# Performance work log

Measured on AMD Instinct MI355X. Metric: run time of the kernel, lower is better.

## Reference

```python
import jax, jax.numpy as jnp
import numpy as np


def setup_inputs() -> dict:
    key = jax.random.key(0)
    ks = jax.random.split(key, 4)
    B, T, I, H, O = 1024, 512, 64, 128, 10
    return {
        "x": jax.random.normal(ks[0], (B, T, I), dtype=jnp.float32),
        "W_hx": jax.random.normal(ks[1], (H, I), dtype=jnp.float32) * (6.0 / (H + I)) ** 0.5,
        "W_hh": jax.random.normal(ks[2], (H, H), dtype=jnp.float32) * (6.0 / (H + H)) ** 0.5,
        "b_hh": jnp.zeros((H,), dtype=jnp.float32),
        "W_ph": jax.random.normal(ks[3], (O, H), dtype=jnp.float32) * (6.0 / (O + H)) ** 0.5,
        "b_ph": jnp.zeros((O,), dtype=jnp.float32),
    }


def reference(x, W_hx, W_hh, b_hh, W_ph, b_ph):
    B, T, I = x.shape
    H = W_hh.shape[0]
    # Precompute input projections for all timesteps in one GEMM: [B,T,H]
    xproj = jnp.einsum("bti,hi->bth", x, W_hx)
    h0 = jnp.zeros((B, H), dtype=x.dtype)

    def step(h, xp_t):
        # xp_t: [B,H]; recurrent update h = tanh(W_hx x_t + W_hh h + b)
        h_new = jnp.tanh(xp_t + h @ W_hh.T + b_hh)
        return h_new, None

    # scan over time (leading axis): xproj transposed to [T,B,H]
    h_T, _ = jax.lax.scan(step, h0, jnp.swapaxes(xproj, 0, 1))
    return h_T @ W_ph.T + b_ph
```

## Files before the change

kernel.cpp:

```cpp
#include <hip/hip_runtime.h>
#include <math.h>


#define T_STEPS 512
#define I_DIM   64
#define H_DIM   128
#define O_DIM   10
#define BT      16
#define PITCH   136

typedef short  bf16x8 __attribute__((ext_vector_type(8)));
typedef float  f32x4  __attribute__((ext_vector_type(4)));

static __device__ inline short f2bf(float f) {
    union { float f; unsigned u; } v; v.f = f;
    unsigned r = v.u + 0x7FFFu + ((v.u >> 16) & 1u);
    return (short)(r >> 16);
}
static __device__ inline float bf2f(short s) {
    union { unsigned u; float f; } v; v.u = ((unsigned)(unsigned short)s) << 16;
    return v.f;
}

static __device__ inline void lds_barrier() {
    asm volatile("s_waitcnt lgkmcnt(0)\n\ts_barrier" ::: "memory");
}

#define RNN_STEP(t, XR)                                                         \
    {                                                                           \
        const int p = (t) & 1;                                                  \
         \
        const short* hb = hbuf[p] + c * PITCH + q * 8;                          \
        bf16x8 Ah0 = *(const bf16x8*)(hb +  0);                                 \
        bf16x8 Ah1 = *(const bf16x8*)(hb + 32);                                 \
        bf16x8 Ah2 = *(const bf16x8*)(hb + 64);                                 \
        bf16x8 Ah3 = *(const bf16x8*)(hb + 96);                                 \
          \
          \
        bf16x8 Ax0, Ax1;                                                        \
        Ax0[0]=f2bf(XR[0].x); Ax0[1]=f2bf(XR[0].y); Ax0[2]=f2bf(XR[0].z); Ax0[3]=f2bf(XR[0].w); \
        Ax0[4]=f2bf(XR[1].x); Ax0[5]=f2bf(XR[1].y); Ax0[6]=f2bf(XR[1].z); Ax0[7]=f2bf(XR[1].w); \
        Ax1[0]=f2bf(XR[2].x); Ax1[1]=f2bf(XR[2].y); Ax1[2]=f2bf(XR[2].z); Ax1[3]=f2bf(XR[2].w); \
        Ax1[4]=f2bf(XR[3].x); Ax1[5]=f2bf(XR[3].y); Ax1[6]=f2bf(XR[3].z); Ax1[7]=f2bf(XR[3].w); \
        {                                                                       \
            const int tn = ((t) + 2 < T_STEPS) ? (t) + 2 : T_STEPS - 1;         \
            const float* pn = xrow + (size_t)tn * I_DIM;                        \
            XR[0] = *(const float4*)(pn +      q * 8);                          \
            XR[1] = *(const float4*)(pn +      q * 8 + 4);                      \
            XR[2] = *(const float4*)(pn + 32 + q * 8);                          \
            XR[3] = *(const float4*)(pn + 32 + q * 8 + 4);                      \
        }                                                                       \
            \
        f32x4 C0a = {0.f,0.f,0.f,0.f}, C0b = {0.f,0.f,0.f,0.f};                 \
        f32x4 C1a = {0.f,0.f,0.f,0.f}, C1b = {0.f,0.f,0.f,0.f};                 \
        C0a = __builtin_amdgcn_mfma_f32_16x16x32_bf16(Ax0, __builtin_bit_cast(bf16x8, Bw[0][4]), C0a, 0, 0, 0); \
        C1a = __builtin_amdgcn_mfma_f32_16x16x32_bf16(Ax0, __builtin_bit_cast(bf16x8, Bw[1][4]), C1a, 0, 0, 0); \
        C0b = __builtin_amdgcn_mfma_f32_16x16x32_bf16(Ax1, __builtin_bit_cast(bf16x8, Bw[0][5]), C0b, 0, 0, 0); \
        C1b = __builtin_amdgcn_mfma_f32_16x16x32_bf16(Ax1, __builtin_bit_cast(bf16x8, Bw[1][5]), C1b, 0, 0, 0); \
        C0a = __builtin_amdgcn_mfma_f32_16x16x32_bf16(Ah0, __builtin_bit_cast(bf16x8, Bw[0][0]), C0a, 0, 0, 0); \
        C1a = __builtin_amdgcn_mfma_f32_16x16x32_bf16(Ah0, __builtin_bit_cast(bf16x8, Bw[1][0]), C1a, 0, 0, 0); \
        C0b = __builtin_amdgcn_mfma_f32_16x16x32_bf16(Ah1, __builtin_bit_cast(bf16x8, Bw[0][1]), C0b, 0, 0, 0); \
        C1b = __builtin_amdgcn_mfma_f32_16x16x32_bf16(Ah1, __builtin_bit_cast(bf16x8, Bw[1][1]), C1b, 0, 0, 0); \
        C0a = __builtin_amdgcn_mfma_f32_16x16x32_bf16(Ah2, __builtin_bit_cast(bf16x8, Bw[0][2]), C0a, 0, 0, 0); \
        C1a = __builtin_amdgcn_mfma_f32_16x16x32_bf16(Ah2, __builtin_bit_cast(bf16x8, Bw[1][2]), C1a, 0, 0, 0); \
        C0b = __builtin_amdgcn_mfma_f32_16x16x32_bf16(Ah3, __builtin_bit_cast(bf16x8, Bw[0][3]), C0b, 0, 0, 0); \
        C1b = __builtin_amdgcn_mfma_f32_16x16x32_bf16(Ah3, __builtin_bit_cast(bf16x8, Bw[1][3]), C1b, 0, 0, 0); \
        const f32x4 C0 = C0a + C0b;                                             \
        const f32x4 C1 = C1a + C1b;                                             \
              \
        short* hw = hbuf[1 - p];                                                \
        _Pragma("unroll")                                                       \
        for (int r = 0; r < 4; ++r) {                                           \
            const int m = q * 4 + r;                                            \
            float s0 = C0[r] + bias0;                                           \
            float s1 = C1[r] + bias1;                                           \
            float e0 = __builtin_amdgcn_exp2f(s0 * 2.885390081777926825f);      \
            float e1 = __builtin_amdgcn_exp2f(s1 * 2.885390081777926825f);      \
            float h0 = fmaf(-2.0f, __builtin_amdgcn_rcpf(e0 + 1.0f), 1.0f);     \
            float h1 = fmaf(-2.0f, __builtin_amdgcn_rcpf(e1 + 1.0f), 1.0f);     \
            hw[m * PITCH + w * 32 + c]      = f2bf(h0);                         \
            hw[m * PITCH + w * 32 + 16 + c] = f2bf(h1);                         \
        }                                                                       \
        lds_barrier();               \
    }

__global__ __launch_bounds__(256)
__attribute__((amdgpu_waves_per_eu(1, 2)))
void rnn_mfma_kernel(
    const float* __restrict__ x,
    const float* __restrict__ W_hx,
    const float* __restrict__ W_hh,
    const float* __restrict__ b_hh,
    const float* __restrict__ W_ph,
    const float* __restrict__ b_ph,
    float* __restrict__ out)
{
    const int b0   = blockIdx.x * BT;
    const int tid  = threadIdx.x;
    const int w    = tid >> 6;
    const int lane = tid & 63;
    const int c    = lane & 15;
    const int q    = lane >> 4;

    __shared__ short hbuf[2][BT * PITCH];

    int4 Bw[2][6];
    #pragma unroll
    for (int nt = 0; nt < 2; ++nt) {
        const int n = w * 32 + nt * 16 + c;
        #pragma unroll
        for (int kt = 0; kt < 6; ++kt) {
            const float* src = (kt < 4) ? (W_hh + n * H_DIM + kt * 32 + q * 8)
                                        : (W_hx + n * I_DIM + (kt - 4) * 32 + q * 8);
            short e[8];
            #pragma unroll
            for (int j = 0; j < 8; ++j) e[j] = f2bf(src[j]);
            Bw[nt][kt].x = ((int)(unsigned short)e[0]) | ((int)(unsigned short)e[1] << 16);
            Bw[nt][kt].y = ((int)(unsigned short)e[2]) | ((int)(unsigned short)e[3] << 16);
            Bw[nt][kt].z = ((int)(unsigned short)e[4]) | ((int)(unsigned short)e[5] << 16);
            Bw[nt][kt].w = ((int)(unsigned short)e[6]) | ((int)(unsigned short)e[7] << 16);
        }
    }
    #pragma unroll
    for (int nt = 0; nt < 2; ++nt)
        #pragma unroll
        for (int kt = 0; kt < 6; ++kt)
            asm volatile("" : "+v"(Bw[nt][kt].x), "+v"(Bw[nt][kt].y),
                              "+v"(Bw[nt][kt].z), "+v"(Bw[nt][kt].w));

    const float bias0 = b_hh[w * 32 + c];
    const float bias1 = b_hh[w * 32 + 16 + c];

    for (int idx = tid; idx < BT * PITCH; idx += 256) hbuf[0][idx] = 0;

    const float* xrow = x + (size_t)(b0 + c) * T_STEPS * I_DIM;
    float4 xrA[4], xrB[4];
    {
        const float* p0 = xrow;
        xrA[0] = *(const float4*)(p0 +      q * 8);
        xrA[1] = *(const float4*)(p0 +      q * 8 + 4);
        xrA[2] = *(const float4*)(p0 + 32 + q * 8);
        xrA[3] = *(const float4*)(p0 + 32 + q * 8 + 4);
        const float* p1 = xrow + I_DIM;
        xrB[0] = *(const float4*)(p1 +      q * 8);
        xrB[1] = *(const float4*)(p1 +      q * 8 + 4);
        xrB[2] = *(const float4*)(p1 + 32 + q * 8);
        xrB[3] = *(const float4*)(p1 + 32 + q * 8 + 4);
    }
    __syncthreads();

    #pragma unroll 1
    for (int t = 0; t < T_STEPS; t += 2) {
        RNN_STEP(t,     xrA)
        RNN_STEP(t + 1, xrB)
    }

    if (tid < BT * O_DIM) {
        const int m = tid / O_DIM;
        const int o = tid % O_DIM;
        float acc = b_ph[o];
        #pragma unroll 4
        for (int k = 0; k < H_DIM; ++k)
            acc = fmaf(W_ph[o * H_DIM + k], bf2f(hbuf[0][m * PITCH + k]), acc);
        out[(size_t)(b0 + m) * O_DIM + o] = acc;
    }
}

extern "C" void kernel_launch(void* const* d_in, const int* in_sizes, int n_in,
                              void* d_out, int out_size, void* d_ws, size_t ws_size,
                              hipStream_t stream) {
    const float* x    = (const float*)d_in[0];
    const float* W_hx = (const float*)d_in[1];
    const float* W_hh = (const float*)d_in[2];
    const float* b_hh = (const float*)d_in[3];
    const float* W_ph = (const float*)d_in[4];
    const float* b_ph = (const float*)d_in[5];
    float* out = (float*)d_out;

    rnn_mfma_kernel<<<1024 / BT, 256, 0, stream>>>(x, W_hx, W_hh, b_hh, W_ph, b_ph, out);
}
```

Measured before the change: 522.6 us.

## Split hidden dim across eight waves, one 16-column tile per wave

Doubles the block to 512 threads (8 waves) so each wave computes a single 16-column slice of the hidden state instead of two. This halves the per-wave MFMA chain, tanh work and register footprint on the serial recurrence critical path. The cost is more waves participating in every per-step LDS barrier, and each wave now redundantly loads and converts the same x rows. Only 64 blocks exist on a 256-CU device, so per-step latency dominates the run time.

```diff
diff --git a/kernel.cpp b/kernel.cpp
--- a/kernel.cpp
+++ b/kernel.cpp
@@ -8,6 +8,7 @@
 #define O_DIM   10
 #define BT      16
 #define PITCH   136
+#define NTHR    512
 
 typedef short  bf16x8 __attribute__((ext_vector_type(8)));
 typedef float  f32x4  __attribute__((ext_vector_type(4)));
@@ -35,8 +36,6 @@
         bf16x8 Ah1 = *(const bf16x8*)(hb + 32);                                 \
         bf16x8 Ah2 = *(const bf16x8*)(hb + 64);                                 \
         bf16x8 Ah3 = *(const bf16x8*)(hb + 96);                                 \
-          \
-          \
         bf16x8 Ax0, Ax1;                                                        \
         Ax0[0]=f2bf(XR[0].x); Ax0[1]=f2bf(XR[0].y); Ax0[2]=f2bf(XR[0].z); Ax0[3]=f2bf(XR[0].w); \
         Ax0[4]=f2bf(XR[1].x); Ax0[5]=f2bf(XR[1].y); Ax0[6]=f2bf(XR[1].z); Ax0[7]=f2bf(XR[1].w); \
@@ -50,41 +49,29 @@
             XR[2] = *(const float4*)(pn + 32 + q * 8);                          \
             XR[3] = *(const float4*)(pn + 32 + q * 8 + 4);                      \
         }                                                                       \
-            \
-        f32x4 C0a = {0.f,0.f,0.f,0.f}, C0b = {0.f,0.f,0.f,0.f};                 \
-        f32x4 C1a = {0.f,0.f,0.f,0.f}, C1b = {0.f,0.f,0.f,0.f};                 \
-        C0a = __builtin_amdgcn_mfma_f32_16x16x32_bf16(Ax0, __builtin_bit_cast(bf16x8, Bw[0][4]), C0a, 0, 0, 0); \
-        C1a = __builtin_amdgcn_mfma_f32_16x16x32_bf16(Ax0, __builtin_bit_cast(bf16x8, Bw[1][4]), C1a, 0, 0, 0); \
-        C0b = __builtin_amdgcn_mfma_f32_16x16x32_bf16(Ax1, __builtin_bit_cast(bf16x8, Bw[0][5]), C0b, 0, 0, 0); \
-        C1b = __builtin_amdgcn_mfma_f32_16x16x32_bf16(Ax1, __builtin_bit_cast(bf16x8, Bw[1][5]), C1b, 0, 0, 0); \
-        C0a = __builtin_amdgcn_mfma_f32_16x16x32_bf16(Ah0, __builtin_bit_cast(bf16x8, Bw[0][0]), C0a, 0, 0, 0); \
-        C1a = __builtin_amdgcn_mfma_f32_16x16x32_bf16(Ah0, __builtin_bit_cast(bf16x8, Bw[1][0]), C1a, 0, 0, 0); \
-        C0b = __builtin_amdgcn_mfma_f32_16x16x32_bf16(Ah1, __builtin_bit_cast(bf16x8, Bw[0][1]), C0b, 0, 0, 0); \
-        C1b = __builtin_amdgcn_mfma_f32_16x16x32_bf16(Ah1, __builtin_bit_cast(bf16x8, Bw[1][1]), C1b, 0, 0, 0); \
-        C0a = __builtin_amdgcn_mfma_f32_16x16x32_bf16(Ah2, __builtin_bit_cast(bf16x8, Bw[0][2]), C0a, 0, 0, 0); \
-        C1a = __builtin_amdgcn_mfma_f32_16x16x32_bf16(Ah2, __builtin_bit_cast(bf16x8, Bw[1][2]), C1a, 0, 0, 0); \
-        C0b = __builtin_amdgcn_mfma_f32_16x16x32_bf16(Ah3, __builtin_bit_cast(bf16x8, Bw[0][3]), C0b, 0, 0, 0); \
-        C1b = __builtin_amdgcn_mfma_f32_16x16x32_bf16(Ah3, __builtin_bit_cast(bf16x8, Bw[1][3]), C1b, 0, 0, 0); \
-        const f32x4 C0 = C0a + C0b;                                             \
-        const f32x4 C1 = C1a + C1b;                                             \
+                                     \
+        f32x4 Ca = {0.f,0.f,0.f,0.f}, Cb = {0.f,0.f,0.f,0.f};                   \
+        Ca = __builtin_amdgcn_mfma_f32_16x16x32_bf16(Ax0, __builtin_bit_cast(bf16x8, Bw[4]), Ca, 0, 0, 0); \
+        Cb = __builtin_amdgcn_mfma_f32_16x16x32_bf16(Ax1, __builtin_bit_cast(bf16x8, Bw[5]), Cb, 0, 0, 0); \
+        Ca = __builtin_amdgcn_mfma_f32_16x16x32_bf16(Ah0, __builtin_bit_cast(bf16x8, Bw[0]), Ca, 0, 0, 0); \
+        Cb = __builtin_amdgcn_mfma_f32_16x16x32_bf16(Ah1, __builtin_bit_cast(bf16x8, Bw[1]), Cb, 0, 0, 0); \
+        Ca = __builtin_amdgcn_mfma_f32_16x16x32_bf16(Ah2, __builtin_bit_cast(bf16x8, Bw[2]), Ca, 0, 0, 0); \
+        Cb = __builtin_amdgcn_mfma_f32_16x16x32_bf16(Ah3, __builtin_bit_cast(bf16x8, Bw[3]), Cb, 0, 0, 0); \
+        const f32x4 C = Ca + Cb;                                                \
               \
         short* hw = hbuf[1 - p];                                                \
         _Pragma("unroll")                                                       \
         for (int r = 0; r < 4; ++r) {                                           \
             const int m = q * 4 + r;                                            \
-            float s0 = C0[r] + bias0;                                           \
-            float s1 = C1[r] + bias1;                                           \
+            float s0 = C[r] + bias;                                             \
             float e0 = __builtin_amdgcn_exp2f(s0 * 2.885390081777926825f);      \
-            float e1 = __builtin_amdgcn_exp2f(s1 * 2.885390081777926825f);      \
             float h0 = fmaf(-2.0f, __builtin_amdgcn_rcpf(e0 + 1.0f), 1.0f);     \
-            float h1 = fmaf(-2.0f, __builtin_amdgcn_rcpf(e1 + 1.0f), 1.0f);     \
-            hw[m * PITCH + w * 32 + c]      = f2bf(h0);                         \
-            hw[m * PITCH + w * 32 + 16 + c] = f2bf(h1);                         \
+            hw[m * PITCH + w * 16 + c] = f2bf(h0);                              \
         }                                                                       \
         lds_barrier();               \
     }
 
-__global__ __launch_bounds__(256)
+__global__ __launch_bounds__(NTHR)
 __attribute__((amdgpu_waves_per_eu(1, 2)))
 void rnn_mfma_kernel(
     const float* __restrict__ x,
@@ -104,10 +91,9 @@
 
     __shared__ short hbuf[2][BT * PITCH];
 
-    int4 Bw[2][6];
-    #pragma unroll
-    for (int nt = 0; nt < 2; ++nt) {
-        const int n = w * 32 + nt * 16 + c;
+    int4 Bw[6];
+    {
+        const int n = w * 16 + c;
         #pragma unroll
         for (int kt = 0; kt < 6; ++kt) {
             const float* src = (kt < 4) ? (W_hh + n * H_DIM + kt * 32 + q * 8)
@@ -115,23 +101,20 @@
             short e[8];
             #pragma unroll
             for (int j = 0; j < 8; ++j) e[j] = f2bf(src[j]);
-            Bw[nt][kt].x = ((int)(unsigned short)e[0]) | ((int)(unsigned short)e[1] << 16);
-            Bw[nt][kt].y = ((int)(unsigned short)e[2]) | ((int)(unsigned short)e[3] << 16);
-            Bw[nt][kt].z = ((int)(unsigned short)e[4]) | ((int)(unsigned short)e[5] << 16);
-            Bw[nt][kt].w = ((int)(unsigned short)e[6]) | ((int)(unsigned short)e[7] << 16);
+            Bw[kt].x = ((int)(unsigned short)e[0]) | ((int)(unsigned short)e[1] << 16);
+            Bw[kt].y = ((int)(unsigned short)e[2]) | ((int)(unsigned short)e[3] << 16);
+            Bw[kt].z = ((int)(unsigned short)e[4]) | ((int)(unsigned short)e[5] << 16);
+            Bw[kt].w = ((int)(unsigned short)e[6]) | ((int)(unsigned short)e[7] << 16);
         }
     }
     #pragma unroll
-    for (int nt = 0; nt < 2; ++nt)
-        #pragma unroll
-        for (int kt = 0; kt < 6; ++kt)
-            asm volatile("" : "+v"(Bw[nt][kt].x), "+v"(Bw[nt][kt].y),
-                              "+v"(Bw[nt][kt].z), "+v"(Bw[nt][kt].w));
+    for (int kt = 0; kt < 6; ++kt)
+        asm volatile("" : "+v"(Bw[kt].x), "+v"(Bw[kt].y),
+                          "+v"(Bw[kt].z), "+v"(Bw[kt].w));
 
-    const float bias0 = b_hh[w * 32 + c];
-    const float bias1 = b_hh[w * 32 + 16 + c];
+    const float bias = b_hh[w * 16 + c];
 
-    for (int idx = tid; idx < BT * PITCH; idx += 256) hbuf[0][idx] = 0;
+    for (int idx = tid; idx < BT * PITCH; idx += NTHR) hbuf[0][idx] = 0;
 
     const float* xrow = x + (size_t)(b0 + c) * T_STEPS * I_DIM;
     float4 xrA[4], xrB[4];
@@ -177,5 +160,5 @@
     const float* b_ph = (const float*)d_in[5];
     float* out = (float*)d_out;
 
-    rnn_mfma_kernel<<<1024 / BT, 256, 0, stream>>>(x, W_hx, W_hh, b_hh, W_ph, b_ph, out);
+    rnn_mfma_kernel<<<1024 / BT, NTHR, 0, stream>>>(x, W_hx, W_hh, b_hh, W_ph, b_ph, out);
 }
```

Result: slower. 623.7 us (+19.4%).

## Software-pipeline input projection MFMAs one step ahead off the recurrent critical path

Applied to the files above, without the earlier changes.

The W_hx·x_t MFMAs for the next timestep are now issued after the tanh/LDS write of the current step, and their results seed the accumulators of the following recurrent step. This takes the input-projection MFMAs and the bf16 conversion off the serial h-dependency chain so they overlap with the barrier wait. It also replaces the round-to-nearest-even bf16 conversion with a cheaper round-half-up packed conversion, which changes rounding slightly and adds accumulator register pressure.

```diff
diff --git a/kernel.cpp b/kernel.cpp
--- a/kernel.cpp
+++ b/kernel.cpp
@@ -12,11 +12,21 @@
 typedef short  bf16x8 __attribute__((ext_vector_type(8)));
 typedef float  f32x4  __attribute__((ext_vector_type(4)));
 
+#define MFMA(A, Bi, C) __builtin_amdgcn_mfma_f32_16x16x32_bf16((A), __builtin_bit_cast(bf16x8, (Bi)), (C), 0, 0, 0)
+
 static __device__ inline short f2bf(float f) {
     union { float f; unsigned u; } v; v.f = f;
     unsigned r = v.u + 0x7FFFu + ((v.u >> 16) & 1u);
     return (short)(r >> 16);
 }
+static __device__ inline unsigned rbf(float f) {
+    return (__builtin_bit_cast(unsigned, f) + 0x8000u) >> 16;
+}
+static __device__ inline int pk2(float a, float b) {
+    unsigned ua = __builtin_bit_cast(unsigned, a);
+    unsigned ub = __builtin_bit_cast(unsigned, b);
+    return (int)(((ua + 0x8000u) >> 16) | ((ub + 0x8000u) & 0xFFFF0000u));
+}
 static __device__ inline float bf2f(short s) {
     union { unsigned u; float f; } v; v.u = ((unsigned)(unsigned short)s) << 16;
     return v.f;
@@ -26,62 +36,54 @@
     asm volatile("s_waitcnt lgkmcnt(0)\n\ts_barrier" ::: "memory");
 }
 
-#define RNN_STEP(t, XR)                                                         \
+#define RNN_STEP(P, XR, TN)                                                     \
     {                                                                           \
-        const int p = (t) & 1;                                                  \
-         \
-        const short* hb = hbuf[p] + c * PITCH + q * 8;                          \
+        const short* hb = hbuf[P] + c * PITCH + q * 8;                          \
         bf16x8 Ah0 = *(const bf16x8*)(hb +  0);                                 \
         bf16x8 Ah1 = *(const bf16x8*)(hb + 32);                                 \
         bf16x8 Ah2 = *(const bf16x8*)(hb + 64);                                 \
         bf16x8 Ah3 = *(const bf16x8*)(hb + 96);                                 \
-          \
-          \
-        bf16x8 Ax0, Ax1;                                                        \
-        Ax0[0]=f2bf(XR[0].x); Ax0[1]=f2bf(XR[0].y); Ax0[2]=f2bf(XR[0].z); Ax0[3]=f2bf(XR[0].w); \
-        Ax0[4]=f2bf(XR[1].x); Ax0[5]=f2bf(XR[1].y); Ax0[6]=f2bf(XR[1].z); Ax0[7]=f2bf(XR[1].w); \
-        Ax1[0]=f2bf(XR[2].x); Ax1[1]=f2bf(XR[2].y); Ax1[2]=f2bf(XR[2].z); Ax1[3]=f2bf(XR[2].w); \
-        Ax1[4]=f2bf(XR[3].x); Ax1[5]=f2bf(XR[3].y); Ax1[6]=f2bf(XR[3].z); Ax1[7]=f2bf(XR[3].w); \
+        f32x4 Ca0 = Cxa0, Cb0 = Cxb0, Ca1 = Cxa1, Cb1 = Cxb1;                   \
+        Ca0 = MFMA(Ah0, Bw[0][0], Ca0); Ca1 = MFMA(Ah0, Bw[1][0], Ca1);         \
+        Cb0 = MFMA(Ah1, Bw[0][1], Cb0); Cb1 = MFMA(Ah1, Bw[1][1], Cb1);         \
+        Ca0 = MFMA(Ah2, Bw[0][2], Ca0); Ca1 = MFMA(Ah2, Bw[1][2], Ca1);         \
+        Cb0 = MFMA(Ah3, Bw[0][3], Cb0); Cb1 = MFMA(Ah3, Bw[1][3], Cb1);         \
+        const f32x4 C0 = Ca0 + Cb0;                                             \
+        const f32x4 C1 = Ca1 + Cb1;                                             \
+        short* hw = hbuf[1 - (P)];                                              \
+        _Pragma("unroll")                                                       \
+        for (int r = 0; r < 4; ++r) {                                           \
+            const int m = q * 4 + r;                                            \
+            float s0 = C0[r] + bias0, s1 = C1[r] + bias1;                       \
+            float e0 = __builtin_amdgcn_exp2f(s0 * 2.885390081777926825f);      \
+            float e1 = __builtin_amdgcn_exp2f(s1 * 2.885390081777926825f);      \
+            float h0 = fmaf(-2.0f, __builtin_amdgcn_rcpf(e0 + 1.0f), 1.0f);     \
+            float h1 = fmaf(-2.0f, __builtin_amdgcn_rcpf(e1 + 1.0f), 1.0f);     \
+            hw[m * PITCH + w * 32 + c]      = (short)rbf(h0);                   \
+            hw[m * PITCH + w * 32 + 16 + c] = (short)rbf(h1);                   \
+        }                                                                       \
+         \
         {                                                                       \
-            const int tn = ((t) + 2 < T_STEPS) ? (t) + 2 : T_STEPS - 1;         \
+            int4 axi0, axi1;                                                    \
+            axi0.x = pk2(XR[0].x, XR[0].y); axi0.y = pk2(XR[0].z, XR[0].w);     \
+            axi0.z = pk2(XR[1].x, XR[1].y); axi0.w = pk2(XR[1].z, XR[1].w);     \
+            axi1.x = pk2(XR[2].x, XR[2].y); axi1.y = pk2(XR[2].z, XR[2].w);     \
+            axi1.z = pk2(XR[3].x, XR[3].y); axi1.w = pk2(XR[3].z, XR[3].w);     \
+            const int tn = ((TN) < T_STEPS) ? (TN) : (T_STEPS - 1);             \
             const float* pn = xrow + (size_t)tn * I_DIM;                        \
             XR[0] = *(const float4*)(pn +      q * 8);                          \
             XR[1] = *(const float4*)(pn +      q * 8 + 4);                      \
             XR[2] = *(const float4*)(pn + 32 + q * 8);                          \
             XR[3] = *(const float4*)(pn + 32 + q * 8 + 4);                      \
+            bf16x8 Ax0 = __builtin_bit_cast(bf16x8, axi0);                      \
+            bf16x8 Ax1 = __builtin_bit_cast(bf16x8, axi1);                      \
+            const f32x4 Z = {0.f, 0.f, 0.f, 0.f};                               \
+            Cxa0 = MFMA(Ax0, Bw[0][4], Z);                                      \
+            Cxb0 = MFMA(Ax1, Bw[0][5], Z);                                      \
+            Cxa1 = MFMA(Ax0, Bw[1][4], Z);                                      \
+            Cxb1 = MFMA(Ax1, Bw[1][5], Z);                                      \
         }                                                                       \
-            \
-        f32x4 C0a = {0.f,0.f,0.f,0.f}, C0b = {0.f,0.f,0.f,0.f};                 \
-        f32x4 C1a = {0.f,0.f,0.f,0.f}, C1b = {0.f,0.f,0.f,0.f};                 \
-        C0a = __builtin_amdgcn_mfma_f32_16x16x32_bf16(Ax0, __builtin_bit_cast(bf16x8, Bw[0][4]), C0a, 0, 0, 0); \
-        C1a = __builtin_amdgcn_mfma_f32_16x16x32_bf16(Ax0, __builtin_bit_cast(bf16x8, Bw[1][4]), C1a, 0, 0, 0); \
-        C0b = __builtin_amdgcn_mfma_f32_16x16x32_bf16(Ax1, __builtin_bit_cast(bf16x8, Bw[0][5]), C0b, 0, 0, 0); \
-        C1b = __builtin_amdgcn_mfma_f32_16x16x32_bf16(Ax1, __builtin_bit_cast(bf16x8, Bw[1][5]), C1b, 0, 0, 0); \
-        C0a = __builtin_amdgcn_mfma_f32_16x16x32_bf16(Ah0, __builtin_bit_cast(bf16x8, Bw[0][0]), C0a, 0, 0, 0); \
-        C1a = __builtin_amdgcn_mfma_f32_16x16x32_bf16(Ah0, __builtin_bit_cast(bf16x8, Bw[1][0]), C1a, 0, 0, 0); \
-        C0b = __builtin_amdgcn_mfma_f32_16x16x32_bf16(Ah1, __builtin_bit_cast(bf16x8, Bw[0][1]), C0b, 0, 0, 0); \
-        C1b = __builtin_amdgcn_mfma_f32_16x16x32_bf16(Ah1, __builtin_bit_cast(bf16x8, Bw[1][1]), C1b, 0, 0, 0); \
-        C0a = __builtin_amdgcn_mfma_f32_16x16x32_bf16(Ah2, __builtin_bit_cast(bf16x8, Bw[0][2]), C0a, 0, 0, 0); \
-        C1a = __builtin_amdgcn_mfma_f32_16x16x32_bf16(Ah2, __builtin_bit_cast(bf16x8, Bw[1][2]), C1a, 0, 0, 0); \
-        C0b = __builtin_amdgcn_mfma_f32_16x16x32_bf16(Ah3, __builtin_bit_cast(bf16x8, Bw[0][3]), C0b, 0, 0, 0); \
-        C1b = __builtin_amdgcn_mfma_f32_16x16x32_bf16(Ah3, __builtin_bit_cast(bf16x8, Bw[1][3]), C1b, 0, 0, 0); \
-        const f32x4 C0 = C0a + C0b;                                             \
-        const f32x4 C1 = C1a + C1b;                                             \
-              \
-        short* hw = hbuf[1 - p];                                                \
-        _Pragma("unroll")                                                       \
-        for (int r = 0; r < 4; ++r) {                                           \
-            const int m = q * 4 + r;                                            \
-            float s0 = C0[r] + bias0;                                           \
-            float s1 = C1[r] + bias1;                                           \
-            float e0 = __builtin_amdgcn_exp2f(s0 * 2.885390081777926825f);      \
-            float e1 = __builtin_amdgcn_exp2f(s1 * 2.885390081777926825f);      \
-            float h0 = fmaf(-2.0f, __builtin_amdgcn_rcpf(e0 + 1.0f), 1.0f);     \
-            float h1 = fmaf(-2.0f, __builtin_amdgcn_rcpf(e1 + 1.0f), 1.0f);     \
-            hw[m * PITCH + w * 32 + c]      = f2bf(h0);                         \
-            hw[m * PITCH + w * 32 + 16 + c] = f2bf(h1);                         \
-        }                                                                       \
-        lds_barrier();               \
+        lds_barrier();                                                          \
     }
 
 __global__ __launch_bounds__(256)
@@ -147,12 +149,33 @@
         xrB[2] = *(const float4*)(p1 + 32 + q * 8);
         xrB[3] = *(const float4*)(p1 + 32 + q * 8 + 4);
     }
+
+    f32x4 Cxa0, Cxb0, Cxa1, Cxb1;
+    {
+        int4 axi0, axi1;
+        axi0.x = pk2(xrA[0].x, xrA[0].y); axi0.y = pk2(xrA[0].z, xrA[0].w);
+        axi0.z = pk2(xrA[1].x, xrA[1].y); axi0.w = pk2(xrA[1].z, xrA[1].w);
+        axi1.x = pk2(xrA[2].x, xrA[2].y); axi1.y = pk2(xrA[2].z, xrA[2].w);
+        axi1.z = pk2(xrA[3].x, xrA[3].y); axi1.w = pk2(xrA[3].z, xrA[3].w);
+        const float* p2 = xrow + 2 * I_DIM;
+        xrA[0] = *(const float4*)(p2 +      q * 8);
+        xrA[1] = *(const float4*)(p2 +      q * 8 + 4);
+        xrA[2] = *(const float4*)(p2 + 32 + q * 8);
+        xrA[3] = *(const float4*)(p2 + 32 + q * 8 + 4);
+        bf16x8 Ax0 = __builtin_bit_cast(bf16x8, axi0);
+        bf16x8 Ax1 = __builtin_bit_cast(bf16x8, axi1);
+        const f32x4 Z = {0.f, 0.f, 0.f, 0.f};
+        Cxa0 = MFMA(Ax0, Bw[0][4], Z);
+        Cxb0 = MFMA(Ax1, Bw[0][5], Z);
+        Cxa1 = MFMA(Ax0, Bw[1][4], Z);
+        Cxb1 = MFMA(Ax1, Bw[1][5], Z);
+    }
     __syncthreads();
 
     #pragma unroll 1
     for (int t = 0; t < T_STEPS; t += 2) {
-        RNN_STEP(t,     xrA)
-        RNN_STEP(t + 1, xrB)
+        RNN_STEP(0, xrB, t + 3)
+        RNN_STEP(1, xrA, t + 4)
     }
 
     if (tid < BT * O_DIM) {
```

New measurement: 512.7 us. Within noise of the previous version (-1.9%).
